# Kernel optimization log

Hardware: AMD Instinct MI355X
Metric: run time of the kernel (lower is better)

## Reference

```python
import jax, jax.numpy as jnp
import numpy as np

ALPHA = 0.2  # tf.nn.leaky_relu default

def leaky(x):
    return jnp.where(x >= 0, x, ALPHA * x)

def segment_softmax(score, seg, num_segments):
    m = jax.ops.segment_max(score, seg, num_segments=num_segments)
    e = jnp.exp(score - m[seg])
    denom = jax.ops.segment_sum(e, seg, num_segments=num_segments)
    return e / denom[seg]

def setup_inputs() -> dict:
    key = jax.random.key(0)
    ks = jax.random.split(key, 8)
    E, NE, NR, D, U = 500000, 100000, 1000, 128, 128
    return {
        "h_index": jax.random.randint(ks[0], (E,), 0, NE),
        "r_index": jax.random.randint(ks[1], (E,), 0, NR),
        "t_index": jax.random.randint(ks[2], (E,), 0, NE),
        "entity_embeddings": jax.random.normal(ks[3], (NE, D), jnp.float32),
        "relation_embeddings": jax.random.normal(ks[4], (NR, D), jnp.float32),
        "W": jax.random.normal(ks[5], (3 * D, U), jnp.float32) * 0.05,
        "a": jax.random.normal(ks[6], (U, 1), jnp.float32) * 0.1,
        "a_b": jnp.zeros((1,), jnp.float32),
        "bias": jnp.zeros((U,), jnp.float32),
    }

def reference(h_index, r_index, t_index, entity_embeddings, relation_embeddings, W, a, a_b, bias):
    num_entities = entity_embeddings.shape[0]
    h = entity_embeddings[h_index]          # [E, D]
    r = relation_embeddings[r_index]        # [E, D]
    t = entity_embeddings[t_index]          # [E, D]
    feats = jnp.concatenate([h, r, t], axis=-1) @ W  # [E, U]
    # att_kernel Dense(1, activation=leaky_relu), then wrapped again in att_activation
    score = leaky(leaky(feats @ a + a_b))[:, 0]      # [E]
    alpha = segment_softmax(score, h_index, num_entities)
    msg = feats * alpha[:, None]                     # gcn_mapper: edge features * weight
    reduced = jax.ops.segment_sum(msg, h_index, num_segments=num_entities)  # [NE, U]
    out = reduced + bias                             # identity_updater returns reduced_msg
    return jax.nn.relu(out)
```

## Files before the change

kernel.cpp:

```cpp
#include <hip/hip_runtime.h>
#include <hip/hip_bf16.h>

#define ALPHA2 0.04f

typedef __attribute__((ext_vector_type(8))) short short8;
typedef __attribute__((ext_vector_type(4))) float floatx4;
typedef __attribute__((ext_vector_type(8))) unsigned short ushort8;

__device__ __forceinline__ unsigned short f2bf(float f) {
    unsigned u = __float_as_uint(f);
    unsigned r = (u + 0x7fffu + ((u >> 16) & 1u)) >> 16;
    return (unsigned short)r;
}
__device__ __forceinline__ float bf2f(unsigned short h) {
    return __uint_as_float((unsigned)h << 16);
}

__device__ __forceinline__ void async_copy16(const float* g, float* lds_base) {
    __builtin_amdgcn_global_load_lds(
        (const __attribute__((address_space(1))) unsigned int*)g,
        (__attribute__((address_space(3))) unsigned int*)lds_base, 16, 0, 0);
}


__global__ void k_prep(const float* __restrict__ W, unsigned short* __restrict__ Bfr,
                       int* __restrict__ count, int NE) {
    int idx = blockIdx.x * blockDim.x + threadIdx.x;
    if (idx < 3 * 128 * 128) {
        int kk = idx & 7, n = (idx >> 3) & 127, g = idx >> 10;
        int slice = g >> 4, kc = (g >> 2) & 3, quad = g & 3;
        int k = kc * 32 + quad * 8 + kk;
        Bfr[idx] = f2bf(W[(size_t)(slice * 128 + k) * 128 + n]);
    }
    if (idx < NE) count[idx] = 0;
}

__global__ __launch_bounds__(256, 4) void k_gemm_all(
        const float* __restrict__ ent, const float* __restrict__ rel,
        const unsigned short* __restrict__ Bfr,
        unsigned short* __restrict__ Pb, unsigned short* __restrict__ Qb,
        unsigned short* __restrict__ Rb,
        float* __restrict__ s1, float* __restrict__ s3, float* __restrict__ s2,
        const float* __restrict__ avec, int NE, int NR, int NBcnt, int NBent,
        const int* __restrict__ hidx, int* __restrict__ count,
        int* __restrict__ rank, int E) {
    __shared__ __align__(16) float Ash[64 * 128];
    int tid = threadIdx.x;
    int b = blockIdx.x;

    if (b < NBcnt) {
        int e = b * 256 + tid;
        if (e < E) rank[e] = atomicAdd(count + hidx[e], 1);
        return;
    }
    int gb = b - NBcnt;

    bool isEnt = gb < NBent;
    const float* In = isEnt ? ent : rel;
    int nrows = isEnt ? NE : NR;
    int rowbase = (isEnt ? gb : gb - NBent) * 64;

    int wave = tid >> 6, lane = tid & 63;

    #pragma unroll
    for (int i = 0; i < 8; ++i) {
        int r = wave * 16 + i * 2 + (lane >> 5);
        int grow = rowbase + r;
        if (grow > nrows - 1) grow = nrows - 1;
        int c = (lane & 31) ^ (r & 7);
        async_copy16(In + (size_t)grow * 128 + c * 4,
                     Ash + (size_t)(wave * 16 + i * 2) * 128);
    }
    __syncthreads();

    int m16 = lane & 15, quad = lane >> 4;
    int rs = wave * 16;
    int R = rs + m16, sw = R & 7;
    const float4* rowp = (const float4*)(Ash + (size_t)R * 128);

    float av[8];
    #pragma unroll
    for (int j = 0; j < 8; ++j) av[j] = avec[j * 16 + m16];

    int nphase = isEnt ? 2 : 1;
    for (int ph = 0; ph < nphase; ++ph) {
        int slice; unsigned short* Out; float* svec;
        if (isEnt) { slice = ph ? 2 : 0; Out = ph ? Qb : Pb; svec = ph ? s3 : s1; }
        else       { slice = 1; Out = Rb; svec = s2; }

        floatx4 acc[8];
        #pragma unroll
        for (int j = 0; j < 8; ++j) acc[j] = (floatx4){0.f, 0.f, 0.f, 0.f};

        short8 bf0[8], bf1[8];
        auto loadB = [&](int kc, short8* dst) {
            const unsigned short* bb =
                Bfr + (size_t)((slice * 4 + kc) * 4 + quad) * 1024 + m16 * 8;
            #pragma unroll
            for (int j = 0; j < 8; ++j) dst[j] = *(const short8*)(bb + j * 128);
        };
        auto doMfma = [&](int kc, short8* bf) {
            int c0 = kc * 8 + quad * 2;
            float4 fa = rowp[c0 ^ sw];
            float4 fb = rowp[(c0 + 1) ^ sw];
            short8 af;
            af[0] = (short)f2bf(fa.x); af[1] = (short)f2bf(fa.y);
            af[2] = (short)f2bf(fa.z); af[3] = (short)f2bf(fa.w);
            af[4] = (short)f2bf(fb.x); af[5] = (short)f2bf(fb.y);
            af[6] = (short)f2bf(fb.z); af[7] = (short)f2bf(fb.w);
            #pragma unroll
            for (int j = 0; j < 8; ++j)
                acc[j] = __builtin_amdgcn_mfma_f32_16x16x32_bf16(af, bf[j], acc[j], 0, 0, 0);
        };
        loadB(0, bf0);
        loadB(1, bf1);
        doMfma(0, bf0);
        loadB(2, bf0);
        doMfma(1, bf1);
        loadB(3, bf1);
        doMfma(2, bf0);
        doMfma(3, bf1);

        #pragma unroll
        for (int reg = 0; reg < 4; ++reg) {
            int row = rowbase + rs + quad * 4 + reg;
            float part = 0.f;
            ushort8 v;
            #pragma unroll
            for (int j = 0; j < 8; ++j) {
                float x = acc[j][reg];
                part = fmaf(x, av[j], part);
                v[j] = f2bf(x);
            }
            #pragma unroll
            for (int off = 1; off < 16; off <<= 1) part += __shfl_xor(part, off);
            if (row < nrows) {
                *(ushort8*)(Out + (size_t)row * 128 + m16 * 8) = v;
                if (m16 == 0) svec[row] = part;
            }
        }
    }
}

__device__ __forceinline__ int block_incl_scan256(int s, int* sh, int t) {
    sh[t] = s; __syncthreads();
    #pragma unroll
    for (int off = 1; off < 256; off <<= 1) {
        int x = 0;
        if (t >= off) x = sh[t - off];
        __syncthreads();
        sh[t] += x;
        __syncthreads();
    }
    return sh[t];
}

__global__ __launch_bounds__(256) void k_scan_a(const int* __restrict__ count, int NE,
                                                int* __restrict__ bsum) {
    __shared__ int sh[256];
    int b = blockIdx.x, t = threadIdx.x;
    int base = b * 1024 + t * 4, s = 0;
    #pragma unroll
    for (int j = 0; j < 4; ++j) { int i = base + j; if (i < NE) s += count[i]; }
    sh[t] = s; __syncthreads();
    for (int off = 128; off > 0; off >>= 1) {
        if (t < off) sh[t] += sh[t + off];
        __syncthreads();
    }
    if (t == 0) bsum[b] = sh[0];
}

__global__ __launch_bounds__(256) void k_scan_c(const int* __restrict__ count, int NE,
                                                const int* __restrict__ bsum, int NB,
                                                int* __restrict__ rowstart, int E) {
    __shared__ int sh[256];
    int b = blockIdx.x, t = threadIdx.x;
    int sb = (t < NB) ? bsum[t] : 0;
    (void)block_incl_scan256(sb, sh, t);
    int base0 = (b == 0) ? 0 : sh[b - 1];
    __syncthreads();
    int base = b * 1024 + t * 4;
    int v[4]; int s = 0;
    #pragma unroll
    for (int j = 0; j < 4; ++j) { int i = base + j; v[j] = (i < NE) ? count[i] : 0; s += v[j]; }
    int incl = block_incl_scan256(s, sh, t);
    int excl = base0 + incl - s;
    #pragma unroll
    for (int j = 0; j < 4; ++j) {
        int i = base + j;
        if (i < NE) { rowstart[i] = excl; excl += v[j]; }
    }
    if (b == 0 && t == 0) rowstart[NE] = E;
}

__global__ void k_scatter_rt(const int* __restrict__ h, const int* __restrict__ r,
                             const int* __restrict__ t,
                             const int* __restrict__ rowstart,
                             const int* __restrict__ rank,
                             unsigned* __restrict__ rt, int E) {
    int e = blockIdx.x * blockDim.x + threadIdx.x;
    if (e >= E) return;
    rt[rowstart[h[e]] + rank[e]] = ((unsigned)r[e] << 17) | (unsigned)t[e];
}

__global__ __launch_bounds__(256) void k_aggregate(const int* __restrict__ rowstart,
                                                   const unsigned* __restrict__ rt,
                                                   const unsigned short* __restrict__ Pb,
                                                   const unsigned short* __restrict__ Qb,
                                                   const unsigned short* __restrict__ Rb,
                                                   const float* __restrict__ s1,
                                                   const float* __restrict__ s2,
                                                   const float* __restrict__ s3,
                                                   const float* __restrict__ a_b,
                                                   const float* __restrict__ bias,
                                                   float* __restrict__ out, int NE) {
    int gid = blockIdx.x * blockDim.x + threadIdx.x;
    int n = gid >> 4;
    int sl = gid & 15;
    if (n >= NE) return;
    int start = rowstart[n], end = rowstart[n + 1];
    int c0 = sl * 8;
    float base = s1[n] + a_b[0];
    float acc[8] = {};
    float evsum = 0.f;
    int i = start;
    for (; i + 4 <= end; i += 4) {
        unsigned u0 = rt[i], u1 = rt[i + 1], u2 = rt[i + 2], u3 = rt[i + 3];
        unsigned t0 = u0 & 0x1FFFFu, r0i = u0 >> 17;
        unsigned t1 = u1 & 0x1FFFFu, r1i = u1 >> 17;
        unsigned t2 = u2 & 0x1FFFFu, r2i = u2 >> 17;
        unsigned t3 = u3 & 0x1FFFFu, r3i = u3 >> 17;
        ushort8 q0 = *(const ushort8*)(Qb + (size_t)t0 * 128 + c0);
        ushort8 rr0 = *(const ushort8*)(Rb + (size_t)r0i * 128 + c0);
        ushort8 q1 = *(const ushort8*)(Qb + (size_t)t1 * 128 + c0);
        ushort8 rr1 = *(const ushort8*)(Rb + (size_t)r1i * 128 + c0);
        ushort8 q2 = *(const ushort8*)(Qb + (size_t)t2 * 128 + c0);
        ushort8 rr2 = *(const ushort8*)(Rb + (size_t)r2i * 128 + c0);
        ushort8 q3 = *(const ushort8*)(Qb + (size_t)t3 * 128 + c0);
        ushort8 rr3 = *(const ushort8*)(Rb + (size_t)r3i * 128 + c0);
        float x0 = base + s2[r0i] + s3[t0];
        float x1 = base + s2[r1i] + s3[t1];
        float x2 = base + s2[r2i] + s3[t2];
        float x3 = base + s2[r3i] + s3[t3];
        x0 = (x0 >= 0.f) ? x0 : ALPHA2 * x0;
        x1 = (x1 >= 0.f) ? x1 : ALPHA2 * x1;
        x2 = (x2 >= 0.f) ? x2 : ALPHA2 * x2;
        x3 = (x3 >= 0.f) ? x3 : ALPHA2 * x3;
        float ev0 = __expf(x0), ev1 = __expf(x1);
        float ev2 = __expf(x2), ev3 = __expf(x3);
        evsum += (ev0 + ev1) + (ev2 + ev3);
        #pragma unroll
        for (int j = 0; j < 8; ++j) {
            acc[j] = fmaf(ev0, bf2f(q0[j]) + bf2f(rr0[j]), acc[j]);
            acc[j] = fmaf(ev1, bf2f(q1[j]) + bf2f(rr1[j]), acc[j]);
            acc[j] = fmaf(ev2, bf2f(q2[j]) + bf2f(rr2[j]), acc[j]);
            acc[j] = fmaf(ev3, bf2f(q3[j]) + bf2f(rr3[j]), acc[j]);
        }
    }
    for (; i < end; ++i) {
        unsigned u0 = rt[i];
        unsigned t0 = u0 & 0x1FFFFu, r0i = u0 >> 17;
        ushort8 q0 = *(const ushort8*)(Qb + (size_t)t0 * 128 + c0);
        ushort8 rr0 = *(const ushort8*)(Rb + (size_t)r0i * 128 + c0);
        float x0 = base + s2[r0i] + s3[t0];
        x0 = (x0 >= 0.f) ? x0 : ALPHA2 * x0;
        float ev0 = __expf(x0);
        evsum += ev0;
        #pragma unroll
        for (int j = 0; j < 8; ++j)
            acc[j] = fmaf(ev0, bf2f(q0[j]) + bf2f(rr0[j]), acc[j]);
    }
    float bi[8];
    #pragma unroll
    for (int j = 0; j < 8; ++j) bi[j] = bias[j * 16 + sl];
    float o[8];
    if (end > start) {
        float inv = 1.f / evsum;
        ushort8 pb = *(const ushort8*)(Pb + (size_t)n * 128 + c0);
        #pragma unroll
        for (int j = 0; j < 8; ++j) o[j] = bf2f(pb[j]) + acc[j] * inv + bi[j];
    } else {
        #pragma unroll
        for (int j = 0; j < 8; ++j) o[j] = bi[j];
    }
    #pragma unroll
    for (int j = 0; j < 8; ++j)
        out[(size_t)n * 128 + j * 16 + sl] = fmaxf(o[j], 0.f);
}

static inline size_t align_up(size_t x, size_t a) { return (x + a - 1) / a * a; }

extern "C" void kernel_launch(void* const* d_in, const int* in_sizes, int n_in,
                              void* d_out, int out_size, void* d_ws, size_t ws_size,
                              hipStream_t stream) {
    const int* h_index = (const int*)d_in[0];
    const int* r_index = (const int*)d_in[1];
    const int* t_index = (const int*)d_in[2];
    const float* ent = (const float*)d_in[3];
    const float* rel = (const float*)d_in[4];
    const float* W = (const float*)d_in[5];
    const float* a = (const float*)d_in[6];
    const float* a_b = (const float*)d_in[7];
    const float* bias = (const float*)d_in[8];
    float* out = (float*)d_out;

    int E = in_sizes[0];
    int NE = in_sizes[3] / 128;
    int NR = in_sizes[4] / 128;

    char* p = (char*)d_ws;
    auto alloc = [&](size_t bytes) { char* q = p; p += align_up(bytes, 256); return (void*)q; };
    unsigned short* Pb = (unsigned short*)alloc((size_t)NE * 128 * 2);
    unsigned short* Qb = (unsigned short*)alloc((size_t)NE * 128 * 2);
    unsigned short* Rb = (unsigned short*)alloc((size_t)NR * 128 * 2);
    unsigned short* Bfr = (unsigned short*)alloc((size_t)3 * 128 * 128 * 2);
    float* s1 = (float*)alloc((size_t)NE * 4);
    float* s3 = (float*)alloc((size_t)NE * 4);
    float* s2 = (float*)alloc((size_t)NR * 4);
    int* count = (int*)alloc((size_t)NE * 4);
    int* rowstart = (int*)alloc((size_t)(NE + 1) * 4);
    int* rank = (int*)alloc((size_t)E * 4);
    int NB = (NE + 1023) / 1024;
    int* bsum = (int*)alloc((size_t)NB * 4);
    unsigned* rt = (unsigned*)alloc((size_t)E * 4);
    (void)ws_size; (void)n_in; (void)out_size;

    int nprep = (NE > 3 * 128 * 128) ? NE : 3 * 128 * 128;
    k_prep<<<(nprep + 255) / 256, 256, 0, stream>>>(W, Bfr, count, NE);
    int NBent = (NE + 63) / 64, NBrel = (NR + 63) / 64;
    int NBcnt = (E + 255) / 256;
    k_gemm_all<<<NBcnt + NBent + NBrel, 256, 0, stream>>>(
        ent, rel, Bfr, Pb, Qb, Rb, s1, s3, s2, a, NE, NR, NBcnt, NBent,
        h_index, count, rank, E);
    k_scan_a<<<NB, 256, 0, stream>>>(count, NE, bsum);
    k_scan_c<<<NB, 256, 0, stream>>>(count, NE, bsum, NB, rowstart, E);
    k_scatter_rt<<<(E + 255) / 256, 256, 0, stream>>>(h_index, r_index, t_index,
                                                      rowstart, rank, rt, E);
    k_aggregate<<<(NE * 16 + 255) / 256, 256, 0, stream>>>(rowstart, rt, Pb, Qb, Rb,
                                                           s1, s2, s3, a_b, bias,
                                                           out, NE);
}
```

Baseline: 202.8 us.

## Merge two-pass scan into single-pass lookback scan and interleave counting blocks

Replaces the two scan kernels with one kernel in which each block publishes its tile sum through a flag-tagged 64-bit state and waits on the sums of all earlier blocks. This removes a kernel launch and a second read of the counts. The edge-counting atomics now use 1024 edges per block, and those blocks are spread evenly among the GEMM blocks so the atomics overlap with the matrix work. The cross-block spin-wait assumes earlier blocks are resident or already done, which holds for the small grid of about 98 blocks.

```diff
diff --git a/kernel.cpp b/kernel.cpp
--- a/kernel.cpp
+++ b/kernel.cpp
@@ -24,7 +24,8 @@
 
 
 __global__ void k_prep(const float* __restrict__ W, unsigned short* __restrict__ Bfr,
-                       int* __restrict__ count, int NE) {
+                       int* __restrict__ count, int NE,
+                       unsigned long long* __restrict__ tstate, int NBt) {
     int idx = blockIdx.x * blockDim.x + threadIdx.x;
     if (idx < 3 * 128 * 128) {
         int kk = idx & 7, n = (idx >> 3) & 127, g = idx >> 10;
@@ -33,6 +34,7 @@
         Bfr[idx] = f2bf(W[(size_t)(slice * 128 + k) * 128 + n]);
     }
     if (idx < NE) count[idx] = 0;
+    if (idx < NBt) tstate[idx] = 0ull;
 }
 
 __global__ __launch_bounds__(256, 4) void k_gemm_all(
@@ -42,18 +44,25 @@
         unsigned short* __restrict__ Rb,
         float* __restrict__ s1, float* __restrict__ s3, float* __restrict__ s2,
         const float* __restrict__ avec, int NE, int NR, int NBcnt, int NBent,
+        int total,
         const int* __restrict__ hidx, int* __restrict__ count,
         int* __restrict__ rank, int E) {
     __shared__ __align__(16) float Ash[64 * 128];
     int tid = threadIdx.x;
     int b = blockIdx.x;
 
-    if (b < NBcnt) {
-        int e = b * 256 + tid;
-        if (e < E) rank[e] = atomicAdd(count + hidx[e], 1);
+    int cb_before = (int)(((long long)b * NBcnt) / total);
+    int cb_after = (int)(((long long)(b + 1) * NBcnt) / total);
+    if (cb_after > cb_before) {
+        int base_e = cb_before * 1024;
+        #pragma unroll
+        for (int k2 = 0; k2 < 4; ++k2) {
+            int e = base_e + k2 * 256 + tid;
+            if (e < E) rank[e] = atomicAdd(count + hidx[e], 1);
+        }
         return;
     }
-    int gb = b - NBcnt;
+    int gb = b - cb_after;
 
     bool isEnt = gb < NBent;
     const float* In = isEnt ? ent : rel;
@@ -155,36 +164,37 @@
     return sh[t];
 }
 
-__global__ __launch_bounds__(256) void k_scan_a(const int* __restrict__ count, int NE,
-                                                int* __restrict__ bsum) {
+__global__ __launch_bounds__(256) void k_scan1(const int* __restrict__ count, int NE,
+                                               unsigned long long* __restrict__ tstate,
+                                               int* __restrict__ rowstart, int E) {
     __shared__ int sh[256];
     int b = blockIdx.x, t = threadIdx.x;
-    int base = b * 1024 + t * 4, s = 0;
-    #pragma unroll
-    for (int j = 0; j < 4; ++j) { int i = base + j; if (i < NE) s += count[i]; }
-    sh[t] = s; __syncthreads();
+    int base = b * 1024 + t * 4;
+    int v[4]; int s = 0;
+    #pragma unroll
+    for (int j = 0; j < 4; ++j) { int i = base + j; v[j] = (i < NE) ? count[i] : 0; s += v[j]; }
+    int incl = block_incl_scan256(s, sh, t);
+    if (t == 0) {
+        unsigned long long pk = (1ull << 32) | (unsigned)sh[255];
+        __hip_atomic_store(&tstate[b], pk, __ATOMIC_RELEASE, __HIP_MEMORY_SCOPE_AGENT);
+    }
+    int myval = 0;
+    if (t < b) {
+        unsigned long long pk;
+        for (;;) {
+            pk = __hip_atomic_load(&tstate[t], __ATOMIC_ACQUIRE, __HIP_MEMORY_SCOPE_AGENT);
+            if (pk >> 32) break;
+            __builtin_amdgcn_s_sleep(1);
+        }
+        myval = (int)(unsigned)pk;
+    }
+    __syncthreads();
+    sh[t] = myval; __syncthreads();
     for (int off = 128; off > 0; off >>= 1) {
         if (t < off) sh[t] += sh[t + off];
         __syncthreads();
     }
-    if (t == 0) bsum[b] = sh[0];
-}
-
-__global__ __launch_bounds__(256) void k_scan_c(const int* __restrict__ count, int NE,
-                                                const int* __restrict__ bsum, int NB,
-                                                int* __restrict__ rowstart, int E) {
-    __shared__ int sh[256];
-    int b = blockIdx.x, t = threadIdx.x;
-    int sb = (t < NB) ? bsum[t] : 0;
-    (void)block_incl_scan256(sb, sh, t);
-    int base0 = (b == 0) ? 0 : sh[b - 1];
-    __syncthreads();
-    int base = b * 1024 + t * 4;
-    int v[4]; int s = 0;
-    #pragma unroll
-    for (int j = 0; j < 4; ++j) { int i = base + j; v[j] = (i < NE) ? count[i] : 0; s += v[j]; }
-    int incl = block_incl_scan256(s, sh, t);
-    int excl = base0 + incl - s;
+    int excl = sh[0] + incl - s;
     #pragma unroll
     for (int j = 0; j < 4; ++j) {
         int i = base + j;
@@ -321,19 +331,20 @@
     int* rowstart = (int*)alloc((size_t)(NE + 1) * 4);
     int* rank = (int*)alloc((size_t)E * 4);
     int NB = (NE + 1023) / 1024;
-    int* bsum = (int*)alloc((size_t)NB * 4);
+    unsigned long long* tstate = (unsigned long long*)alloc((size_t)NB * 8);
     unsigned* rt = (unsigned*)alloc((size_t)E * 4);
     (void)ws_size; (void)n_in; (void)out_size;
 
     int nprep = (NE > 3 * 128 * 128) ? NE : 3 * 128 * 128;
-    k_prep<<<(nprep + 255) / 256, 256, 0, stream>>>(W, Bfr, count, NE);
+    k_prep<<<(nprep + 255) / 256, 256, 0, stream>>>(W, Bfr, count, NE, tstate, NB);
     int NBent = (NE + 63) / 64, NBrel = (NR + 63) / 64;
-    int NBcnt = (E + 255) / 256;
-    k_gemm_all<<<NBcnt + NBent + NBrel, 256, 0, stream>>>(
-        ent, rel, Bfr, Pb, Qb, Rb, s1, s3, s2, a, NE, NR, NBcnt, NBent,
+    int NBgemm = NBent + NBrel;
+    int NBcnt = (E + 1023) / 1024;
+    int total = NBcnt + NBgemm;
+    k_gemm_all<<<total, 256, 0, stream>>>(
+        ent, rel, Bfr, Pb, Qb, Rb, s1, s3, s2, a, NE, NR, NBcnt, NBent, total,
         h_index, count, rank, E);
-    k_scan_a<<<NB, 256, 0, stream>>>(count, NE, bsum);
-    k_scan_c<<<NB, 256, 0, stream>>>(count, NE, bsum, NB, rowstart, E);
+    k_scan1<<<NB, 256, 0, stream>>>(count, NE, tstate, rowstart, E);
     k_scatter_rt<<<(E + 255) / 256, 256, 0, stream>>>(h_index, r_index, t_index,
                                                       rowstart, rank, rt, E);
     k_aggregate<<<(NE * 16 + 255) / 256, 256, 0, stream>>>(rowstart, rt, Pb, Qb, Rb,
```

New measurement: 190.5 us. -6.0%, faster.
